# Kernel tuning notes

Measured on AMD Instinct MI355X. Metric: run time of the kernel, lower is better.

## Reference

```python
import jax, jax.numpy as jnp
import numpy as np

N_IN, N_HID, N_OUT = 200, 256, 2
BN_EPS = 1e-5


def _mlp(x, W1, b1, W2, b2):
    # two-layer MLP with ELU activations (dropout prob = 0.0 -> omitted)
    h = jax.nn.elu(x @ W1 + b1)
    return jax.nn.elu(h @ W2 + b2)


def _batch_norm(x, gamma, beta):
    # torch BatchNorm1d in training mode over flattened (B*E) rows, biased variance
    m = x.mean(axis=(0, 1))
    v = x.var(axis=(0, 1))
    return (x - m) * jax.lax.rsqrt(v + BN_EPS) * gamma + beta


def setup_inputs() -> dict:
    key = jax.random.key(0)
    ks = jax.random.split(key, 12)
    B, N, T, D = 32, 100, 50, 4
    inputs = jax.random.normal(ks[0], (B, N, T, D), dtype=jnp.float32)
    # one-hot receiver/sender matrices over all N*(N-1) ordered off-diagonal pairs
    idx = np.array([(i, j) for i in range(N) for j in range(N) if i != j])
    eye = np.eye(N, dtype=np.float32)
    rel_rec = jnp.asarray(eye[idx[:, 0]])   # [E, N]
    rel_send = jnp.asarray(eye[idx[:, 1]])  # [E, N]

    def lin(k, fi, fo):  # xavier_normal weight
        std = float(np.sqrt(2.0 / (fi + fo)))
        return jax.random.normal(k, (fi, fo), dtype=jnp.float32) * std

    b = lambda n: jnp.full((n,), 0.1, dtype=jnp.float32)
    return dict(
        inputs=inputs, rel_rec=rel_rec, rel_send=rel_send,
        mlp1_W1=lin(ks[1], N_IN, N_HID), mlp1_b1=b(N_HID),
        mlp1_W2=lin(ks[2], N_HID, N_HID), mlp1_b2=b(N_HID),
        mlp2_W1=lin(ks[3], 2 * N_HID, N_HID), mlp2_b1=b(N_HID),
        mlp2_W2=lin(ks[4], N_HID, N_HID), mlp2_b2=b(N_HID),
        mlp3_W1=lin(ks[5], N_HID, N_HID), mlp3_b1=b(N_HID),
        mlp3_W2=lin(ks[6], N_HID, N_HID), mlp3_b2=b(N_HID),
        mlp4_W1=lin(ks[7], 3 * N_HID, N_HID), mlp4_b1=b(N_HID),
        mlp4_W2=lin(ks[8], N_HID, N_HID), mlp4_b2=b(N_HID),
        mlp4_bn_gamma=jnp.ones((N_HID,), jnp.float32),
        mlp4_bn_beta=jnp.zeros((N_HID,), jnp.float32),
        fc_W=lin(ks[9], N_HID, N_OUT), fc_b=b(N_OUT),
    )


def reference(inputs, rel_rec, rel_send,
              mlp1_W1, mlp1_b1, mlp1_W2, mlp1_b2,
              mlp2_W1, mlp2_b1, mlp2_W2, mlp2_b2,
              mlp3_W1, mlp3_b1, mlp3_W2, mlp3_b2,
              mlp4_W1, mlp4_b1, mlp4_W2, mlp4_b2,
              mlp4_bn_gamma, mlp4_bn_beta, fc_W, fc_b):
    B, N = inputs.shape[0], inputs.shape[1]
    x = inputs.reshape(B, N, -1)                       # [B, N, T*D]
    x = _mlp(x, mlp1_W1, mlp1_b1, mlp1_W2, mlp1_b2)     # [B, N, H]

    def node2edge(h):
        recv = jnp.einsum('en,bnh->beh', rel_rec, h)
        send = jnp.einsum('en,bnh->beh', rel_send, h)
        return jnp.concatenate([send, recv], axis=2)    # [B, E, 2H]

    x = node2edge(x)
    x = _mlp(x, mlp2_W1, mlp2_b1, mlp2_W2, mlp2_b2)     # [B, E, H]
    x_skip = x
    # factor=True branch
    incoming = jnp.einsum('en,beh->bnh', rel_rec, x) / x.shape[1]  # edge2node, /N per code
    x = _mlp(incoming, mlp3_W1, mlp3_b1, mlp3_W2, mlp3_b2)
    x = node2edge(x)                                    # [B, E, 2H]
    x = jnp.concatenate([x, x_skip], axis=2)            # [B, E, 3H]
    x = _mlp(x, mlp4_W1, mlp4_b1, mlp4_W2, mlp4_b2)
    x = _batch_norm(x, mlp4_bn_gamma, mlp4_bn_beta)
    return x @ fc_W + fc_b                              # [B, E, n_out]
```

## Files before the change

### kernel.cpp

```cpp
#include <hip/hip_runtime.h>
#include <math.h>


typedef unsigned short ushort_t;
typedef __bf16 bf16x8 __attribute__((ext_vector_type(8)));
typedef float  f32x4  __attribute__((ext_vector_type(4)));

#define E_EDGES 9900
#define NNODE   100
#define HID     256
#define M_BIG   316800
#define M_SMALL 3200
#define NBLK2   (M_BIG / 128)

__device__ __forceinline__ float bf2f(ushort_t u) {
    union { unsigned int i; float f; } v; v.i = ((unsigned int)u) << 16; return v.f;
}
__device__ __forceinline__ ushort_t f2bf(float f) {
    union { __bf16 h; ushort_t u; } v; v.h = (__bf16)f; return v.u;
}
__device__ __forceinline__ float elu_f(float x) {
    return x > 0.f ? x : (__expf(x) - 1.f);
}

__global__ __launch_bounds__(256)
void wcvt_all(const float* __restrict__ s0, const float* __restrict__ s1,
              const float* __restrict__ s2, const float* __restrict__ s3,
              const float* __restrict__ s4, const float* __restrict__ s5,
              const float* __restrict__ s6, const float* __restrict__ s7,
              ushort_t* d0, ushort_t* d1, ushort_t* d2, ushort_t* d3,
              ushort_t* d4, ushort_t* d5, ushort_t* d6, ushort_t* d7)
{
    int bid = blockIdx.x;
    const float* S; ushort_t* D; int Kd, Kr, t;
    if      (bid < 16)  { S = s0; D = d0; Kd = 256; Kr = 200; t = bid; }
    else if (bid < 32)  { S = s1; D = d1; Kd = 256; Kr = 256; t = bid - 16; }
    else if (bid < 64)  { S = s2; D = d2; Kd = 512; Kr = 512; t = bid - 32; }
    else if (bid < 80)  { S = s3; D = d3; Kd = 256; Kr = 256; t = bid - 64; }
    else if (bid < 96)  { S = s4; D = d4; Kd = 256; Kr = 256; t = bid - 80; }
    else if (bid < 112) { S = s5; D = d5; Kd = 256; Kr = 256; t = bid - 96; }
    else if (bid < 160) { S = s6; D = d6; Kd = 768; Kr = 768; t = bid - 112; }
    else                { S = s7; D = d7; Kd = 256; Kr = 256; t = bid - 160; }
    int k0 = (t >> 2) * 64, c0 = (t & 3) * 64;
    __shared__ float Sh[64][65];
    int tid = threadIdx.x;
    #pragma unroll
    for (int i = 0; i < 16; ++i) {
        int idx = tid + i * 256;
        int kk = idx >> 6, cc = idx & 63;
        Sh[kk][cc] = (k0 + kk < Kr) ? S[(size_t)(k0 + kk) * 256 + c0 + cc] : 0.f;
    }
    __syncthreads();
    int col = tid & 63;
    int kb  = (tid >> 6) * 16;
    ushort_t* dst = D + (size_t)(c0 + col) * Kd + k0 + kb;
    #pragma unroll
    for (int jj = 0; jj < 4; ++jj) {
        ushort4 u;
        u.x = f2bf(Sh[kb + 4 * jj + 0][col]);
        u.y = f2bf(Sh[kb + 4 * jj + 1][col]);
        u.z = f2bf(Sh[kb + 4 * jj + 2][col]);
        u.w = f2bf(Sh[kb + 4 * jj + 3][col]);
        *(ushort4*)(dst + 4 * jj) = u;
    }
}

__device__ __forceinline__ void gemm32(const ushort_t S[32][264],
                                       const ushort_t* __restrict__ WT,
                                       int wstr, int kcn,
                                       int w, int ln15, int klane,
                                       f32x4 acc[2][4])
{
    #pragma unroll
    for (int r = 0; r < 2; ++r)
        #pragma unroll
        for (int c = 0; c < 4; ++c)
            acc[r][c][0] = acc[r][c][1] = acc[r][c][2] = acc[r][c][3] = 0.f;
    int wch[4];
    #pragma unroll
    for (int c = 0; c < 4; ++c) wch[c] = (w * 64 + 16 * c + ln15) * wstr;
    bf16x8 wf0[4];
    #pragma unroll
    for (int c = 0; c < 4; ++c)
        wf0[c] = *(const bf16x8*)(WT + wch[c] + klane);
    for (int kc = 0; kc < kcn; ++kc) {
        bf16x8 wf1[4];
        if (kc + 1 < kcn) {
            #pragma unroll
            for (int c = 0; c < 4; ++c)
                wf1[c] = *(const bf16x8*)(WT + wch[c] + (kc + 1) * 32 + klane);
        }
        bf16x8 af[2];
        #pragma unroll
        for (int r = 0; r < 2; ++r)
            af[r] = *(const bf16x8*)&S[16 * r + ln15][kc * 32 + klane];
        #pragma unroll
        for (int r = 0; r < 2; ++r)
            #pragma unroll
            for (int c = 0; c < 4; ++c)
                acc[r][c] = __builtin_amdgcn_mfma_f32_16x16x32_bf16(wf0[c], af[r], acc[r][c], 0, 0, 0);
        #pragma unroll
        for (int c = 0; c < 4; ++c) wf0[c] = wf1[c];
    }
}

__device__ __forceinline__ void park32(ushort_t D[32][264], f32x4 acc[2][4],
                                       const float* __restrict__ bias,
                                       int act, int w, int ln15, int q)
{
    #pragma unroll
    for (int c = 0; c < 4; ++c) {
        float4 bv = bias ? *(const float4*)&bias[w * 64 + 16 * c + 4 * q]
                         : make_float4(0.f, 0.f, 0.f, 0.f);
        #pragma unroll
        for (int r = 0; r < 2; ++r) {
            float o0 = acc[r][c][0] + bv.x;
            float o1 = acc[r][c][1] + bv.y;
            float o2 = acc[r][c][2] + bv.z;
            float o3 = acc[r][c][3] + bv.w;
            if (act) { o0 = elu_f(o0); o1 = elu_f(o1); o2 = elu_f(o2); o3 = elu_f(o3); }
            ushort4 u;
            u.x = f2bf(o0); u.y = f2bf(o1); u.z = f2bf(o2); u.w = f2bf(o3);
            *(ushort4*)&D[16 * r + ln15][w * 64 + 16 * c + 4 * q] = u;
        }
    }
}

__global__ __launch_bounds__(256, 4)
void mlp_pq(const float* __restrict__ Xf, const float* __restrict__ Xf2,
            int Kreal, int kcN, float xscale,
            const ushort_t* __restrict__ W1T, const float* __restrict__ b1,
            const ushort_t* __restrict__ W2T, const float* __restrict__ b2,
            const ushort_t* __restrict__ WPT, int wsPQ,
            const float* __restrict__ bP, ushort_t* __restrict__ Pout,
            const ushort_t* __restrict__ WQT, ushort_t* __restrict__ Qout)
{
    __shared__ ushort_t Abuf[32][264];
    __shared__ ushort_t Bbuf[32][264];
    const int tid = threadIdx.x;
    const int w = tid >> 6;
    const int l = tid & 63;
    const int ln15 = l & 15;
    const int q = l >> 4;
    const int klane = 8 * q;
    const int half = blockIdx.x >= (int)(gridDim.x >> 1);
    const int blk  = half ? blockIdx.x - (int)(gridDim.x >> 1) : blockIdx.x;
    const int Rbase = blk * 32;

    {
        int row = tid >> 3, seg = tid & 7;
        if (seg < kcN) {
            ushort_t tmp[32];
            const float* src  = Xf + (size_t)(Rbase + row) * Kreal + seg * 32;
            const float* src2 = Xf2 ? Xf2 + (size_t)(Rbase + row) * Kreal + seg * 32
                                    : (const float*)nullptr;
            #pragma unroll
            for (int u = 0; u < 32; ++u) {
                float a = 0.f;
                if (seg * 32 + u < Kreal) {
                    a = src[u];
                    if (Xf2) a += src2[u];
                }
                tmp[u] = f2bf(a * xscale);
            }
            #pragma unroll
            for (int u = 0; u < 4; ++u)
                *(uint4*)&Abuf[row][seg * 32 + u * 8] = *(uint4*)&tmp[u * 8];
        }
    }
    __syncthreads();

    f32x4 acc[2][4];
    gemm32(Abuf, W1T, 256, kcN, w, ln15, klane, acc);
    park32(Bbuf, acc, b1, 1, w, ln15, q);
    __syncthreads();
    gemm32(Bbuf, W2T, 256, 8, w, ln15, klane, acc);
    park32(Abuf, acc, b2, 1, w, ln15, q);
    __syncthreads();

    const ushort_t* WT = half ? WQT : WPT;
    ushort_t* Out = half ? Qout : Pout;
    gemm32(Abuf, WT, wsPQ, 8, w, ln15, klane, acc);
    park32(Bbuf, acc, half ? nullptr : bP, 0, w, ln15, q);
    __syncthreads();
    #pragma unroll
    for (int m = 0; m < 4; ++m) {
        int ch = tid + m * 256;
        int row = ch >> 5;
        int o = (ch & 31) * 8;
        *(uint4*)&Out[(size_t)(Rbase + row) * 256 + o] = *(const uint4*)&Bbuf[row][o];
    }
}

__device__ __forceinline__ void wf0_load(const ushort_t* __restrict__ WT,
                                         int wstr, int w, int ln15, int klane,
                                         bf16x8 wf0[2])
{
    #pragma unroll
    for (int c = 0; c < 2; ++c)
        wf0[c] = *(const bf16x8*)(WT + (w * 32 + 16 * c + ln15) * wstr + klane);
}

__device__ __forceinline__ void gemm128cs(const ushort_t As[128][264],
                                          const ushort_t* __restrict__ WT,
                                          int wstr, int w, int ln15, int klane,
                                          bf16x8 wf0[2], f32x4 acc[8][2])
{
    #pragma unroll
    for (int r = 0; r < 8; ++r)
        #pragma unroll
        for (int c = 0; c < 2; ++c)
            acc[r][c][0] = acc[r][c][1] = acc[r][c][2] = acc[r][c][3] = 0.f;
    int wch[2];
    #pragma unroll
    for (int c = 0; c < 2; ++c) wch[c] = (w * 32 + 16 * c + ln15) * wstr;
    #pragma unroll
    for (int kc = 0; kc < 8; ++kc) {
        bf16x8 wf1[2];
        if (kc < 7) {
            #pragma unroll
            for (int c = 0; c < 2; ++c)
                wf1[c] = *(const bf16x8*)(WT + wch[c] + (kc + 1) * 32 + klane);
        }
        #pragma unroll
        for (int g = 0; g < 2; ++g) {
            bf16x8 af[4];
            #pragma unroll
            for (int r = 0; r < 4; ++r)
                af[r] = *(const bf16x8*)&As[16 * (4 * g + r) + ln15][kc * 32 + klane];
            #pragma unroll
            for (int r = 0; r < 4; ++r)
                #pragma unroll
                for (int c = 0; c < 2; ++c)
                    acc[4 * g + r][c] = __builtin_amdgcn_mfma_f32_16x16x32_bf16(wf0[c], af[r], acc[4 * g + r][c], 0, 0, 0);
        }
        #pragma unroll
        for (int c = 0; c < 2; ++c) wf0[c] = wf1[c];
    }
}

__global__ __launch_bounds__(512, 4)
void edge_mlp2(const ushort_t* __restrict__ Pb, const ushort_t* __restrict__ Qb,
               const ushort_t* __restrict__ W2T,
               const float* __restrict__ b2,
               ushort_t* __restrict__ Y,
               float* __restrict__ part0, float* __restrict__ part1)
{
    __shared__ ushort_t As[128][264];
    __shared__ float Sc2[4][768];
    const int tid = threadIdx.x;
    const int w = tid >> 6;
    const int l = tid & 63;
    const int ln15 = l & 15;
    const int q = l >> 4;
    const int klane = 8 * q;
    const int Rbase = blockIdx.x * 128;

    {
        int row = tid >> 2;
        int R = Rbase + row;
        int b = R / E_EDGES;
        int e = R - b * E_EDGES;
        int i = e / 99;
        int k = e - 99 * i;
        int j = k + (k >= i ? 1 : 0);
        const ushort_t* prow = Pb + (size_t)(b * NNODE + j) * HID;
        const ushort_t* qrow = Qb + (size_t)(b * NNODE + i) * HID;
        int off = (tid & 3) * 8;
        uint4 pv[8], qv[8];
        #pragma unroll
        for (int u = 0; u < 8; ++u) {
            int o = off + u * 32;
            pv[u] = *(const uint4*)(prow + o);
            qv[u] = *(const uint4*)(qrow + o);
        }
        #pragma unroll
        for (int u = 0; u < 8; ++u) {
            int o = off + u * 32;
            union { uint4 v; ushort_t s[8]; } pu, qu, hu;
            pu.v = pv[u]; qu.v = qv[u];
            #pragma unroll
            for (int x = 0; x < 8; ++x)
                hu.s[x] = f2bf(elu_f(bf2f(pu.s[x]) + bf2f(qu.s[x])));
            *(uint4*)&As[row][o] = hu.v;
        }
    }
    bf16x8 wf0[2];
    wf0_load(W2T, 256, w, ln15, klane, wf0);
    __syncthreads();

    f32x4 acc[8][2];
    gemm128cs(As, W2T, 256, w, ln15, klane, wf0, acc);
    __syncthreads();

    #pragma unroll
    for (int c = 0; c < 2; ++c) {
        float4 bv = *(const float4*)&b2[w * 32 + 16 * c + 4 * q];
        #pragma unroll
        for (int r = 0; r < 8; ++r) {
            ushort4 u;
            u.x = f2bf(elu_f(acc[r][c][0] + bv.x));
            u.y = f2bf(elu_f(acc[r][c][1] + bv.y));
            u.z = f2bf(elu_f(acc[r][c][2] + bv.z));
            u.w = f2bf(elu_f(acc[r][c][3] + bv.w));
            *(ushort4*)&As[16 * r + ln15][w * 32 + 16 * c + 4 * q] = u;
        }
    }
    __syncthreads();

    #pragma unroll
    for (int m = 0; m < 8; ++m) {
        int ch = tid + m * 512;
        int row = ch >> 5;
        int o = (ch & 31) * 8;
        *(uint4*)&Y[((size_t)(Rbase + row)) * 256 + o] = *(const uint4*)&As[row][o];
    }

    const int g0   = Rbase / 99;
    const int off0 = Rbase - g0 * 99;
    const int t1   = 99 - off0;
    const int t2   = t1 + 99;
    if (w < 4) {
        int c4 = l * 4;
        float cA[4] = {0.f, 0.f, 0.f, 0.f};
        float cB[4] = {0.f, 0.f, 0.f, 0.f};
        float cC[4] = {0.f, 0.f, 0.f, 0.f};
        for (int r = w * 32; r < w * 32 + 32; ++r) {
            union { ushort4 v; ushort_t e4[4]; } u;
            u.v = *(const ushort4*)&As[r][c4];
            float m1 = (r >= t1) ? 1.f : 0.f;
            float m2 = (r >= t2) ? 1.f : 0.f;
            #pragma unroll
            for (int g = 0; g < 4; ++g) {
                float v = bf2f(u.e4[g]);
                cA[g] += v;
                cB[g] = fmaf(m1, v, cB[g]);
                cC[g] = fmaf(m2, v, cC[g]);
            }
        }
        #pragma unroll
        for (int g = 0; g < 4; ++g) {
            Sc2[w][c4 + g]       = cA[g];
            Sc2[w][256 + c4 + g] = cB[g];
            Sc2[w][512 + c4 + g] = cC[g];
        }
    }
    __syncthreads();
    if (tid < 256) {
        float A = Sc2[0][tid] + Sc2[1][tid] + Sc2[2][tid] + Sc2[3][tid];
        float B = Sc2[0][256 + tid] + Sc2[1][256 + tid] + Sc2[2][256 + tid] + Sc2[3][256 + tid];
        float C = Sc2[0][512 + tid] + Sc2[1][512 + tid] + Sc2[2][512 + tid] + Sc2[3][512 + tid];
        float* d0 = (off0 != 0) ? part1 : part0;
        d0[(size_t)g0 * 256 + tid] = A - B;
        part0[(size_t)(g0 + 1) * 256 + tid] = B - C;
        if (t2 < 128)
            part0[(size_t)(g0 + 2) * 256 + tid] = C;
    }
}

__global__ __launch_bounds__(512, 4)
void edge_mlp4(const ushort_t* __restrict__ Pb, const ushort_t* __restrict__ Qb,
               const ushort_t* __restrict__ X2,
               const ushort_t* __restrict__ WaT, int wsA,
               const ushort_t* __restrict__ WbT, int wsB,
               const float* __restrict__ b2,
               ushort_t* __restrict__ Y, ushort_t* __restrict__ pstat)
{
    __shared__ ushort_t As[128][264];
    __shared__ float Sc[4][512];
    const int tid = threadIdx.x;
    const int w = tid >> 6;
    const int l = tid & 63;
    const int ln15 = l & 15;
    const int q = l >> 4;
    const int klane = 8 * q;
    const int Rbase = blockIdx.x * 128;

    {
        int row = tid >> 2;
        const ushort_t* xrow = X2 + (size_t)(Rbase + row) * 256;
        int off = (tid & 3) * 8;
        uint4 xv[8];
        #pragma unroll
        for (int u = 0; u < 8; ++u) xv[u] = *(const uint4*)(xrow + off + u * 32);
        #pragma unroll
        for (int u = 0; u < 8; ++u) *(uint4*)&As[row][off + u * 32] = xv[u];
    }
    bf16x8 wfa[2];
    wf0_load(WaT, wsA, w, ln15, klane, wfa);
    __syncthreads();

    f32x4 acc[8][2];
    gemm128cs(As, WaT, wsA, w, ln15, klane, wfa, acc);

    int oP[8], oQ[8];
    #pragma unroll
    for (int r = 0; r < 8; ++r) {
        int R = Rbase + 16 * r + ln15;
        int b = R / E_EDGES;
        int e = R - b * E_EDGES;
        int i = e / 99;
        int k = e - 99 * i;
        int j = k + (k >= i ? 1 : 0);
        oP[r] = (b * NNODE + j) * HID;
        oQ[r] = (b * NNODE + i) * HID;
    }
    __syncthreads();

    #pragma unroll
    for (int c = 0; c < 2; ++c) {
        int ch = w * 32 + 16 * c + 4 * q;
        ushort4 pv[8], qv[8];
        #pragma unroll
        for (int r = 0; r < 8; ++r) {
            pv[r] = *(const ushort4*)(Pb + oP[r] + ch);
            qv[r] = *(const ushort4*)(Qb + oQ[r] + ch);
        }
        #pragma unroll
        for (int r = 0; r < 8; ++r) {
            union { ushort4 v; ushort_t s[4]; } pu, qu;
            pu.v = pv[r]; qu.v = qv[r];
            ushort4 u;
            u.x = f2bf(elu_f(acc[r][c][0] + bf2f(pu.s[0]) + bf2f(qu.s[0])));
            u.y = f2bf(elu_f(acc[r][c][1] + bf2f(pu.s[1]) + bf2f(qu.s[1])));
            u.z = f2bf(elu_f(acc[r][c][2] + bf2f(pu.s[2]) + bf2f(qu.s[2])));
            u.w = f2bf(elu_f(acc[r][c][3] + bf2f(pu.s[3]) + bf2f(qu.s[3])));
            *(ushort4*)&As[16 * r + ln15][ch] = u;
        }
    }
    bf16x8 wfb[2];
    wf0_load(WbT, wsB, w, ln15, klane, wfb);
    __syncthreads();

    gemm128cs(As, WbT, wsB, w, ln15, klane, wfb, acc);
    __syncthreads();

    #pragma unroll
    for (int c = 0; c < 2; ++c) {
        float4 bv = *(const float4*)&b2[w * 32 + 16 * c + 4 * q];
        #pragma unroll
        for (int r = 0; r < 8; ++r) {
            ushort4 u;
            u.x = f2bf(elu_f(acc[r][c][0] + bv.x));
            u.y = f2bf(elu_f(acc[r][c][1] + bv.y));
            u.z = f2bf(elu_f(acc[r][c][2] + bv.z));
            u.w = f2bf(elu_f(acc[r][c][3] + bv.w));
            *(ushort4*)&As[16 * r + ln15][w * 32 + 16 * c + 4 * q] = u;
        }
    }
    __syncthreads();

    #pragma unroll
    for (int m = 0; m < 8; ++m) {
        int ch = tid + m * 512;
        int row = ch >> 5;
        int o = (ch & 31) * 8;
        *(uint4*)&Y[((size_t)(Rbase + row)) * 256 + o] = *(const uint4*)&As[row][o];
    }

    if (w < 4) {
        int c4 = l * 4;
        float s[4] = {0.f, 0.f, 0.f, 0.f};
        float qq[4] = {0.f, 0.f, 0.f, 0.f};
        for (int r = w * 32; r < w * 32 + 32; ++r) {
            union { ushort4 v; ushort_t e4[4]; } u;
            u.v = *(const ushort4*)&As[r][c4];
            #pragma unroll
            for (int g = 0; g < 4; ++g) {
                float v = bf2f(u.e4[g]);
                s[g] += v;
                qq[g] = fmaf(v, v, qq[g]);
            }
        }
        #pragma unroll
        for (int g = 0; g < 4; ++g) {
            Sc[w][c4 + g]       = s[g];
            Sc[w][256 + c4 + g] = qq[g];
        }
    }
    __syncthreads();
    {
        float v = Sc[0][tid] + Sc[1][tid] + Sc[2][tid] + Sc[3][tid];
        pstat[(size_t)blockIdx.x * 512 + tid] = f2bf(v);
    }
}

__global__ __launch_bounds__(256)
void reduce_stats(const ushort_t* __restrict__ pstat, float* __restrict__ stats)
{
    int c = threadIdx.x;
    float s = 0.f, q = 0.f;
    for (int b = blockIdx.x; b < NBLK2; b += 64) {
        size_t base = (size_t)b * 512;
        s += bf2f(pstat[base + c]);
        q += bf2f(pstat[base + 256 + c]);
    }
    atomicAdd(&stats[c], s);
    atomicAdd(&stats[256 + c], q);
}

__global__ __launch_bounds__(256)
void fold_kernel(const float* __restrict__ stats,
                 const float* __restrict__ gamma, const float* __restrict__ beta,
                 const float* __restrict__ fcW, const float* __restrict__ fcb,
                 float* __restrict__ fold)
{
    __shared__ float red0[256], red1[256];
    int c = threadIdx.x;
    float mean  = stats[c] * (1.f / M_BIG);
    float var   = stats[256 + c] * (1.f / M_BIG) - mean * mean;
    float inv   = rsqrtf(var + 1e-5f);
    float scale = inv * gamma[c];
    float sh    = beta[c] - mean * scale;
    float w0 = fcW[c * 2 + 0], w1 = fcW[c * 2 + 1];
    fold[c * 2 + 0] = scale * w0;
    fold[c * 2 + 1] = scale * w1;
    red0[c] = sh * w0;
    red1[c] = sh * w1;
    __syncthreads();
    for (int off = 128; off > 0; off >>= 1) {
        if (c < off) { red0[c] += red0[c + off]; red1[c] += red1[c + off]; }
        __syncthreads();
    }
    if (c == 0) {
        fold[512] = red0[0] + fcb[0];
        fold[513] = red1[0] + fcb[1];
    }
}

__global__ __launch_bounds__(256)
void final_kernel(const ushort_t* __restrict__ x4, const float* __restrict__ fold,
                  float* __restrict__ out)
{
    int tid  = threadIdx.x;
    int l32  = tid & 31;
    int g    = tid >> 5;
    int R = blockIdx.x * 8 + g;
    int c0 = l32 * 8;
    union { uint4 qv; ushort_t s[8]; } u;
    u.qv = *(const uint4*)(x4 + (size_t)R * 256 + c0);
    float a0 = 0.f, a1 = 0.f;
    #pragma unroll
    for (int j = 0; j < 8; ++j) {
        float v = bf2f(u.s[j]);
        a0 = fmaf(v, fold[(c0 + j) * 2 + 0], a0);
        a1 = fmaf(v, fold[(c0 + j) * 2 + 1], a1);
    }
    #pragma unroll
    for (int off = 16; off > 0; off >>= 1) {
        a0 += __shfl_down(a0, off);
        a1 += __shfl_down(a1, off);
    }
    if (l32 == 0) {
        out[(size_t)R * 2 + 0] = a0 + fold[512];
        out[(size_t)R * 2 + 1] = a1 + fold[513];
    }
}

extern "C" void kernel_launch(void* const* d_in, const int* in_sizes, int n_in,
                              void* d_out, int out_size, void* d_ws, size_t ws_size,
                              hipStream_t stream)
{
    (void)in_sizes; (void)n_in; (void)out_size; (void)ws_size;

    const float* inputs = (const float*)d_in[0];
    const float* m1W1 = (const float*)d_in[3];
    const float* m1b1 = (const float*)d_in[4];
    const float* m1W2 = (const float*)d_in[5];
    const float* m1b2 = (const float*)d_in[6];
    const float* m2W1 = (const float*)d_in[7];
    const float* m2b1 = (const float*)d_in[8];
    const float* m2W2 = (const float*)d_in[9];
    const float* m2b2 = (const float*)d_in[10];
    const float* m3W1 = (const float*)d_in[11];
    const float* m3b1 = (const float*)d_in[12];
    const float* m3W2 = (const float*)d_in[13];
    const float* m3b2 = (const float*)d_in[14];
    const float* m4W1 = (const float*)d_in[15];
    const float* m4b1 = (const float*)d_in[16];
    const float* m4W2 = (const float*)d_in[17];
    const float* m4b2 = (const float*)d_in[18];
    const float* gamma = (const float*)d_in[19];
    const float* beta  = (const float*)d_in[20];
    const float* fcW   = (const float*)d_in[21];
    const float* fcb   = (const float*)d_in[22];
    float* out = (float*)d_out;

    char* ws = (char*)d_ws;
    const size_t BIGB = (size_t)M_BIG * 256 * 2;
    const size_t HB   = (size_t)M_SMALL * 256 * 2;
    const size_t SM4  = (size_t)M_SMALL * 256 * 4;
    ushort_t* bigX     = (ushort_t*)ws;
    ushort_t* pstat    = (ushort_t*)(ws + BIGB);
    float*    part1    = (float*)(ws + BIGB);
    float*    part0    = (float*)(ws + BIGB + 2 * HB);
    ushort_t* Pbuf     = (ushort_t*)(ws + BIGB + 2 * HB + SM4);
    ushort_t* Qbuf     = (ushort_t*)(ws + BIGB + 3 * HB + SM4);
    float*    stats    = (float*)(ws + BIGB + 4 * HB + SM4);
    float*    fold     = stats + 512;
    ushort_t* w1t      = (ushort_t*)(ws + BIGB + 4 * HB + SM4 + 8192);
    ushort_t* w1bt     = w1t  + 256 * 256;
    ushort_t* w2pt     = w1bt + 256 * 256;
    ushort_t* w2t      = w2pt + 256 * 512;
    ushort_t* w3at     = w2t  + 256 * 256;
    ushort_t* w3bt     = w3at + 256 * 256;
    ushort_t* w4pt     = w3bt + 256 * 256;
    ushort_t* w4bt     = w4pt + 256 * 768;

    hipMemsetAsync(stats, 0, 2048, stream);
    hipMemsetAsync(part1, 0, SM4, stream);

    dim3 blk(256);
    dim3 blk512(512);
    wcvt_all<<<176, blk, 0, stream>>>(m1W1, m1W2, m2W1, m2W2, m3W1, m3W2, m4W1, m4W2,
                                      w1t, w1bt, w2pt, w2t, w3at, w3bt, w4pt, w4bt);
    mlp_pq<<<200, blk, 0, stream>>>(inputs, nullptr, 200, 7, 1.f,
                                    w1t, m1b1, w1bt, m1b2,
                                    w2pt, 512, m2b1, Pbuf,
                                    w2pt + 256, Qbuf);
    edge_mlp2<<<NBLK2, blk512, 0, stream>>>(Pbuf, Qbuf, w2t, m2b2, bigX, part0, part1);
    mlp_pq<<<200, blk, 0, stream>>>(part0, part1, 256, 8, 1.f / 9900.f,
                                    w3at, m3b1, w3bt, m3b2,
                                    w4pt, 768, m4b1, Pbuf,
                                    w4pt + 256, Qbuf);
    edge_mlp4<<<NBLK2, blk512, 0, stream>>>(Pbuf, Qbuf, bigX,
                                            w4pt + 512, 768, w4bt, 256,
                                            m4b2, bigX, pstat);
    reduce_stats<<<64, blk, 0, stream>>>(pstat, stats);
    fold_kernel<<<1, blk, 0, stream>>>(stats, gamma, beta, fcW, fcb, fold);
    final_kernel<<<M_BIG / 8, blk, 0, stream>>>(bigX, fold, out);
}
```

Measured before the change: 448.6 us.

## Double edge_mlp4 row tile to 256 rows with 1024-thread blocks

After: 470.2 us. 1.05x slower.

```diff
diff --git a/kernel.cpp b/kernel.cpp
--- a/kernel.cpp
+++ b/kernel.cpp
@@ -12,6 +12,7 @@
 #define M_BIG   316800
 #define M_SMALL 3200
 #define NBLK2   (M_BIG / 128)
+#define NBLK4   ((M_BIG + 255) / 256)
 
 __device__ __forceinline__ float bf2f(ushort_t u) {
     union { unsigned int i; float f; } v; v.i = ((unsigned int)u) << 16; return v.f;
@@ -358,7 +359,7 @@
     }
 }
 
-__global__ __launch_bounds__(512, 4)
+__global__ __launch_bounds__(1024, 4)
 void edge_mlp4(const ushort_t* __restrict__ Pb, const ushort_t* __restrict__ Qb,
                const ushort_t* __restrict__ X2,
                const ushort_t* __restrict__ WaT, int wsA,
@@ -366,19 +367,24 @@
                const float* __restrict__ b2,
                ushort_t* __restrict__ Y, ushort_t* __restrict__ pstat)
 {
-    __shared__ ushort_t As[128][264];
-    __shared__ float Sc[4][512];
+    __shared__ ushort_t As[256][264];
+    __shared__ float Sc[8][512];
     const int tid = threadIdx.x;
     const int w = tid >> 6;
     const int l = tid & 63;
     const int ln15 = l & 15;
     const int q = l >> 4;
     const int klane = 8 * q;
-    const int Rbase = blockIdx.x * 128;
+    const int wr   = w >> 3;
+    const int wsub = w & 7;
+    const int Rbase = blockIdx.x * 256;
+    const int limit = (M_BIG - Rbase < 256) ? (M_BIG - Rbase) : 256;
 
     {
         int row = tid >> 2;
-        const ushort_t* xrow = X2 + (size_t)(Rbase + row) * 256;
+        int rr = Rbase + row;
+        if (rr >= M_BIG) rr = M_BIG - 1;
+        const ushort_t* xrow = X2 + (size_t)rr * 256;
         int off = (tid & 3) * 8;
         uint4 xv[8];
         #pragma unroll
@@ -387,16 +393,18 @@
         for (int u = 0; u < 8; ++u) *(uint4*)&As[row][off + u * 32] = xv[u];
     }
     bf16x8 wfa[2];
-    wf0_load(WaT, wsA, w, ln15, klane, wfa);
-    __syncthreads();
-
+    wf0_load(WaT, wsA, wsub, ln15, klane, wfa);
+    __syncthreads();
+
+    const ushort_t (*Ah)[264] = (const ushort_t (*)[264])&As[wr * 128][0];
     f32x4 acc[8][2];
-    gemm128cs(As, WaT, wsA, w, ln15, klane, wfa, acc);
+    gemm128cs(Ah, WaT, wsA, wsub, ln15, klane, wfa, acc);
 
     int oP[8], oQ[8];
     #pragma unroll
     for (int r = 0; r < 8; ++r) {
-        int R = Rbase + 16 * r + ln15;
+        int R = Rbase + wr * 128 + 16 * r + ln15;
+        if (R >= M_BIG) R = M_BIG - 1;
         int b = R / E_EDGES;
         int e = R - b * E_EDGES;
         int i = e / 99;
@@ -409,7 +417,7 @@
 
     #pragma unroll
     for (int c = 0; c < 2; ++c) {
-        int ch = w * 32 + 16 * c + 4 * q;
+        int ch = wsub * 32 + 16 * c + 4 * q;
         ushort4 pv[8], qv[8];
         #pragma unroll
         for (int r = 0; r < 8; ++r) {
@@ -425,40 +433,44 @@
             u.y = f2bf(elu_f(acc[r][c][1] + bf2f(pu.s[1]) + bf2f(qu.s[1])));
             u.z = f2bf(elu_f(acc[r][c][2] + bf2f(pu.s[2]) + bf2f(qu.s[2])));
             u.w = f2bf(elu_f(acc[r][c][3] + bf2f(pu.s[3]) + bf2f(qu.s[3])));
-            *(ushort4*)&As[16 * r + ln15][ch] = u;
+            *(ushort4*)&As[wr * 128 + 16 * r + ln15][ch] = u;
         }
     }
     bf16x8 wfb[2];
-    wf0_load(WbT, wsB, w, ln15, klane, wfb);
-    __syncthreads();
-
-    gemm128cs(As, WbT, wsB, w, ln15, klane, wfb, acc);
+    wf0_load(WbT, wsB, wsub, ln15, klane, wfb);
+    __syncthreads();
+
+    gemm128cs(Ah, WbT, wsB, wsub, ln15, klane, wfb, acc);
     __syncthreads();
 
     #pragma unroll
     for (int c = 0; c < 2; ++c) {
-        float4 bv = *(const float4*)&b2[w * 32 + 16 * c + 4 * q];
+        float4 bv = *(const float4*)&b2[wsub * 32 + 16 * c + 4 * q];
         #pragma unroll
         for (int r = 0; r < 8; ++r) {
-            ushort4 u;
-            u.x = f2bf(elu_f(acc[r][c][0] + bv.x));
-            u.y = f2bf(elu_f(acc[r][c][1] + bv.y));
-            u.z = f2bf(elu_f(acc[r][c][2] + bv.z));
-            u.w = f2bf(elu_f(acc[r][c][3] + bv.w));
-            *(ushort4*)&As[16 * r + ln15][w * 32 + 16 * c + 4 * q] = u;
+            int row = wr * 128 + 16 * r + ln15;
+            ushort4 u = make_ushort4(0, 0, 0, 0);
+            if (row < limit) {
+                u.x = f2bf(elu_f(acc[r][c][0] + bv.x));
+                u.y = f2bf(elu_f(acc[r][c][1] + bv.y));
+                u.z = f2bf(elu_f(acc[r][c][2] + bv.z));
+                u.w = f2bf(elu_f(acc[r][c][3] + bv.w));
+            }
+            *(ushort4*)&As[row][wsub * 32 + 16 * c + 4 * q] = u;
         }
     }
     __syncthreads();
 
     #pragma unroll
     for (int m = 0; m < 8; ++m) {
-        int ch = tid + m * 512;
+        int ch = tid + m * 1024;
         int row = ch >> 5;
         int o = (ch & 31) * 8;
-        *(uint4*)&Y[((size_t)(Rbase + row)) * 256 + o] = *(const uint4*)&As[row][o];
-    }
-
-    if (w < 4) {
+        if (row < limit)
+            *(uint4*)&Y[((size_t)(Rbase + row)) * 256 + o] = *(const uint4*)&As[row][o];
+    }
+
+    if (w < 8) {
         int c4 = l * 4;
         float s[4] = {0.f, 0.f, 0.f, 0.f};
         float qq[4] = {0.f, 0.f, 0.f, 0.f};
@@ -479,8 +491,9 @@
         }
     }
     __syncthreads();
-    {
-        float v = Sc[0][tid] + Sc[1][tid] + Sc[2][tid] + Sc[3][tid];
+    if (tid < 512) {
+        float v = Sc[0][tid] + Sc[1][tid] + Sc[2][tid] + Sc[3][tid]
+                + Sc[4][tid] + Sc[5][tid] + Sc[6][tid] + Sc[7][tid];
         pstat[(size_t)blockIdx.x * 512 + tid] = f2bf(v);
     }
 }
@@ -490,7 +503,7 @@
 {
     int c = threadIdx.x;
     float s = 0.f, q = 0.f;
-    for (int b = blockIdx.x; b < NBLK2; b += 64) {
+    for (int b = blockIdx.x; b < NBLK4; b += 64) {
         size_t base = (size_t)b * 512;
         s += bf2f(pstat[base + c]);
         q += bf2f(pstat[base + 256 + c]);
@@ -612,6 +625,7 @@
 
     dim3 blk(256);
     dim3 blk512(512);
+    dim3 blk1024(1024);
     wcvt_all<<<176, blk, 0, stream>>>(m1W1, m1W2, m2W1, m2W2, m3W1, m3W2, m4W1, m4W2,
                                       w1t, w1bt, w2pt, w2t, w3at, w3bt, w4pt, w4bt);
     mlp_pq<<<200, blk, 0, stream>>>(inputs, nullptr, 200, 7, 1.f,
@@ -623,9 +637,9 @@
                                     w3at, m3b1, w3bt, m3b2,
                                     w4pt, 768, m4b1, Pbuf,
                                     w4pt + 256, Qbuf);
-    edge_mlp4<<<NBLK2, blk512, 0, stream>>>(Pbuf, Qbuf, bigX,
-                                            w4pt + 512, 768, w4bt, 256,
-                                            m4b2, bigX, pstat);
+    edge_mlp4<<<NBLK4, blk1024, 0, stream>>>(Pbuf, Qbuf, bigX,
+                                             w4pt + 512, 768, w4bt, 256,
+                                             m4b2, bigX, pstat);
     reduce_stats<<<64, blk, 0, stream>>>(pstat, stats);
     fold_kernel<<<1, blk, 0, stream>>>(stats, gamma, beta, fcW, fcb, fold);
     final_kernel<<<M_BIG / 8, blk, 0, stream>>>(bigX, fold, out);
```
